# Kernel tuning notes

Measured on AMD Instinct MI355X. Metric: run time of the kernel, lower is better.

The kernel has to match this reference:

```python
import jax, jax.numpy as jnp
import numpy as np

T_EPS = 1e-07
NUM_CAPSULE = 10
DIM_CAPSULE = 64
ROUTINGS = 5


def squash(x, axis=-1):
    # NOTE: this repo's 'squash' is just norm-division (no s/(1+s) factor)
    s = jnp.sum(x * x, axis=axis, keepdims=True)
    return x / jnp.sqrt(s + T_EPS)


def setup_inputs() -> dict:
    key = jax.random.key(0)
    k1, k2 = jax.random.split(key)
    B, N, D = 128, 512, 300
    M = NUM_CAPSULE * DIM_CAPSULE  # 640
    x = jax.random.normal(k1, (B, N, D), dtype=jnp.float32)
    # xavier_normal for shape (1, D, M): std = sqrt(2/(fan_in+fan_out))
    std = float(np.sqrt(2.0 / (D + M)))
    W = jax.random.normal(k2, (1, D, M), dtype=jnp.float32) * std
    return {"x": x, "W": W}


def reference(x, W):
    B, N, D = x.shape
    # u_hat_vecs: [B, num_capsule(i), input_num_capsule(j), dim_capsule(k)]
    u = jnp.einsum('bnd,dm->bnm', x, W[0])
    u = u.reshape(B, N, NUM_CAPSULE, DIM_CAPSULE).transpose(0, 2, 1, 3)
    b = jnp.zeros((B, NUM_CAPSULE, N), dtype=x.dtype)
    outputs = None
    for i in range(ROUTINGS):
        # softmax over the num_capsule axis (axis=1 of b), matching the
        # permute(0,2,1) -> softmax(dim=2) -> permute back in torch
        c = jax.nn.softmax(b, axis=1)
        outputs = squash(jnp.einsum('bij,bijk->bik', c, u))  # [B, num, dim]
        if i < ROUTINGS - 1:
            b = jnp.einsum('bik,bijk->bij', outputs, u)
    return outputs
```

## Files before the change

### kernel.cpp

```cpp
#include <hip/hip_runtime.h>
#include <hip/hip_bf16.h>
#include <stdint.h>

#define BQ 128
#define NJ 512
#define DD 300
#define NC 10
#define DC 64
#define MM 640
#define KP 320
#define RT 5

typedef __attribute__((ext_vector_type(8))) short short8;
typedef __attribute__((ext_vector_type(4))) float f32x4;


__global__ void k_cast_x(const float* __restrict__ x, __hip_bfloat16* __restrict__ xb) {
    int g = blockIdx.x * 256 + threadIdx.x;
    int row = g / 40, cg2 = g - row * 40;
    const float* src = x + (size_t)row * DD + cg2 * 8;
    float4 a = make_float4(0.f, 0.f, 0.f, 0.f), b4 = a;
    if (cg2 < 37) { a = *(const float4*)src; b4 = *(const float4*)(src + 4); }
    else if (cg2 == 37) { a = *(const float4*)src; }
    union { ushort u[8]; uint4 v; } o;
    float f[8] = {a.x, a.y, a.z, a.w, b4.x, b4.y, b4.z, b4.w};
#pragma unroll
    for (int e = 0; e < 8; ++e) {
        __hip_bfloat16 hh = __float2bfloat16(f[e]);
        o.u[e] = *(ushort*)&hh;
    }
    *(uint4*)(xb + (size_t)row * KP + cg2 * 8) = o.v;
}

__global__ void k_cast_w(const float* __restrict__ w, __hip_bfloat16* __restrict__ wt) {
    int idx = blockIdx.x * 256 + threadIdx.x;
    int m = idx / KP, k = idx - m * KP;
    float v = (k < DD) ? w[(size_t)k * MM + m] : 0.f;
    wt[idx] = __float2bfloat16(v);
}

__global__ void k_zero(float4* __restrict__ p) {
    p[blockIdx.x * 256 + threadIdx.x] = make_float4(0.f, 0.f, 0.f, 0.f);
}


__global__ __launch_bounds__(256)
void k_gemm(const __hip_bfloat16* __restrict__ A,
            const __hip_bfloat16* __restrict__ Bt,
            __hip_bfloat16* __restrict__ C,
            float* __restrict__ su) {
    __shared__ __align__(16) __hip_bfloat16 As[128 * 64];
    __shared__ __align__(16) __hip_bfloat16 Bs[128 * 64];

    const int L  = blockIdx.x;
    const int n0 = ((L >> 3) % 5) * 128;
    const int m0 = ((L / 40) * 8 + (L & 7)) * 128;
    const int t  = threadIdx.x;
    const int w  = t >> 6, lane = t & 63;
    const int wrow = (w >> 1) * 64, wcol = (w & 1) * 64;
    const int quad = lane >> 4, r = lane & 15;

    f32x4 acc[4][4] = {};

    const int srow = t >> 3;
    const int sl   = (t & 7) ^ (srow & 7);
    const __hip_bfloat16* ag = A  + (size_t)(m0 + srow) * KP + sl * 8;
    const __hip_bfloat16* bg = Bt + (size_t)(n0 + srow) * KP + sl * 8;

    for (int kt = 0; kt < KP / 64; ++kt) {
        __syncthreads();
#pragma unroll
        for (int s = 0; s < 4; ++s) {
            __builtin_amdgcn_global_load_lds(
                (const __attribute__((address_space(1))) void*)(ag + (size_t)s * 32 * KP + kt * 64),
                (__attribute__((address_space(3))) void*)(&As[s * 2048 + t * 8]), 16, 0, 0);
            __builtin_amdgcn_global_load_lds(
                (const __attribute__((address_space(1))) void*)(bg + (size_t)s * 32 * KP + kt * 64),
                (__attribute__((address_space(3))) void*)(&Bs[s * 2048 + t * 8]), 16, 0, 0);
        }
        __syncthreads();

#pragma unroll
        for (int hh = 0; hh < 2; ++hh) {
            short8 af[4], bf[4];
#pragma unroll
            for (int mi = 0; mi < 4; ++mi) {
                int rho = wrow + mi * 16 + r;
                int p = (hh * 4 + quad) ^ (rho & 7);
                af[mi] = *(const short8*)&As[rho * 64 + p * 8];
            }
#pragma unroll
            for (int ni = 0; ni < 4; ++ni) {
                int rho = wcol + ni * 16 + r;
                int p = (hh * 4 + quad) ^ (rho & 7);
                bf[ni] = *(const short8*)&Bs[rho * 64 + p * 8];
            }
#pragma unroll
            for (int mi = 0; mi < 4; ++mi)
#pragma unroll
                for (int ni = 0; ni < 4; ++ni)
                    acc[mi][ni] = __builtin_amdgcn_mfma_f32_16x16x32_bf16(
                        af[mi], bf[ni], acc[mi][ni], 0, 0, 0);
        }
    }

#pragma unroll
    for (int mi = 0; mi < 4; ++mi)
#pragma unroll
        for (int ni = 0; ni < 4; ++ni) {
            int col = n0 + wcol + ni * 16 + r;
#pragma unroll
            for (int p = 0; p < 4; ++p) {
                int row = m0 + wrow + mi * 16 + quad * 4 + p;
                C[(size_t)row * MM + col] = __float2bfloat16(acc[mi][ni][p]);
            }
        }

    float cs[4];
#pragma unroll
    for (int ni = 0; ni < 4; ++ni) {
        float s = 0.f;
#pragma unroll
        for (int mi = 0; mi < 4; ++mi)
#pragma unroll
            for (int p = 0; p < 4; ++p) s += acc[mi][ni][p];
        s += __shfl_xor(s, 16, 64);
        s += __shfl_xor(s, 32, 64);
        cs[ni] = s;
    }
    if (quad == 0) {
        int bb = m0 >> 9;
#pragma unroll
        for (int ni = 0; ni < 4; ++ni)
            atomicAdd(&su[(size_t)bb * MM + n0 + wcol + ni * 16 + r], cs[ni]);
    }
}


__global__ __launch_bounds__(512)
void k_pass(const __hip_bfloat16* __restrict__ u, const float* __restrict__ pprev,
            float* __restrict__ pnext, int first) {
    __shared__ __align__(16) float outl[MM];
    __shared__ __align__(16) float pored[8 * 32 * 20];

    const int t   = threadIdx.x;
    const int blk = blockIdx.x;
    const int b   = blk >> 2, q = blk & 3;
    const int w   = t >> 6, lane = t & 63;
    const int jd  = t >> 5, kg = t & 31;

    const ushort* ubase = (const ushort*)u
        + (size_t)(b * NJ + q * 128 + jd) * MM + kg * 2;

    uint uv[10];
#pragma unroll
    for (int i = 0; i < 10; ++i) uv[i] = *(const uint*)(ubase + i * 64);

    if (w < 5) {
        float s0, s1;
        if (first) {
            s0 = 0.1f * pprev[(size_t)b * MM + w * 64 + lane];
            s1 = 0.1f * pprev[(size_t)b * MM + 320 + w * 64 + lane];
        } else {
            const float* pp = pprev + (size_t)b * 4 * MM;
            s0 = 0.f; s1 = 0.f;
#pragma unroll
            for (int qq = 0; qq < 4; ++qq) {
                s0 += pp[qq * MM + w * 64 + lane];
                s1 += pp[qq * MM + 320 + w * 64 + lane];
            }
        }
        float q0 = s0 * s0, q1 = s1 * s1;
#pragma unroll
        for (int m = 32; m >= 1; m >>= 1) {
            q0 += __shfl_xor(q0, m, 64);
            q1 += __shfl_xor(q1, m, 64);
        }
        outl[w * 64 + lane]       = s0 * rsqrtf(q0 + 1e-7f);
        outl[320 + w * 64 + lane] = s1 * rsqrtf(q1 + 1e-7f);
    }
    __syncthreads();

    float2 oo[10];
#pragma unroll
    for (int i = 0; i < 10; ++i) oo[i] = *(const float2*)(&outl[i * 64 + kg * 2]);

    float po[20];
#pragma unroll
    for (int e = 0; e < 20; ++e) po[e] = 0.f;

    for (int tt = 0; tt < 8; ++tt) {
        uint nv[10];
        if (tt < 7) {
            const ushort* nrow = ubase + (size_t)(tt + 1) * 16 * MM;
#pragma unroll
            for (int i = 0; i < 10; ++i) nv[i] = *(const uint*)(nrow + i * 64);
        }

        float bl[10];
#pragma unroll
        for (int i = 0; i < 10; ++i) {
            float u0 = __uint_as_float(uv[i] << 16);
            float u1 = __uint_as_float(uv[i] & 0xffff0000u);
            bl[i] = u0 * oo[i].x + u1 * oo[i].y;
        }
#pragma unroll
        for (int m = 1; m <= 16; m <<= 1)
#pragma unroll
            for (int i = 0; i < 10; ++i) bl[i] += __shfl_xor(bl[i], m, 64);

        float mx = -1e30f;
#pragma unroll
        for (int i = 0; i < 10; ++i) mx = fmaxf(mx, bl[i]);
        float ssum = 0.f;
#pragma unroll
        for (int i = 0; i < 10; ++i) { bl[i] = __expf(bl[i] - mx); ssum += bl[i]; }
        float inv = 1.f / ssum;

#pragma unroll
        for (int i = 0; i < 10; ++i) {
            float cc = bl[i] * inv;
            float u0 = __uint_as_float(uv[i] << 16);
            float u1 = __uint_as_float(uv[i] & 0xffff0000u);
            po[i * 2 + 0] += cc * u0;
            po[i * 2 + 1] += cc * u1;
        }

        if (tt < 7) {
#pragma unroll
            for (int i = 0; i < 10; ++i) uv[i] = nv[i];
        }
    }

#pragma unroll
    for (int e = 0; e < 20; ++e) po[e] += __shfl_xor(po[e], 32, 64);
    if (lane < 32) {
#pragma unroll
        for (int e = 0; e < 20; ++e) pored[(w * 32 + kg) * 20 + e] = po[e];
    }
    __syncthreads();
    for (int m = t; m < MM; m += 512) {
        int i = m >> 6, k = m & 63, kg2 = k >> 1, kd = k & 1;
        float s = 0.f;
#pragma unroll
        for (int ww = 0; ww < 8; ++ww) s += pored[(ww * 32 + kg2) * 20 + i * 2 + kd];
        pnext[(size_t)blk * MM + m] = s;
    }
}

__global__ __launch_bounds__(640)
void k_squash(const float* __restrict__ pbuf, float* __restrict__ dst) {
    int b = blockIdx.x, t = threadIdx.x;
    float s = 0.f;
#pragma unroll
    for (int qq = 0; qq < 4; ++qq) s += pbuf[(size_t)(b * 4 + qq) * MM + t];
    float sq = s * s;
#pragma unroll
    for (int m = 32; m >= 1; m >>= 1) sq += __shfl_xor(sq, m, 64);
    dst[(size_t)b * MM + t] = s * rsqrtf(sq + 1e-7f);
}


extern "C" void kernel_launch(void* const* d_in, const int* in_sizes, int n_in,
                              void* d_out, int out_size, void* d_ws, size_t ws_size,
                              hipStream_t stream) {
    const float* x = (const float*)d_in[0];
    const float* W = (const float*)d_in[1];
    float* out = (float*)d_out;

    char* ws = (char*)d_ws;
    size_t o = 0;
    __hip_bfloat16* xb = (__hip_bfloat16*)(ws + o); o += (size_t)BQ * NJ * KP * 2;
    __hip_bfloat16* wt = (__hip_bfloat16*)(ws + o); o += (size_t)MM * KP * 2;
    __hip_bfloat16* u  = (__hip_bfloat16*)(ws + o); o += (size_t)BQ * NJ * MM * 2;
    float* pb0 = (float*)(ws + o); o += (size_t)512 * MM * 4;
    float* pb1 = (float*)(ws + o); o += (size_t)512 * MM * 4;
    float* su  = (float*)(ws + o); o += (size_t)BQ * MM * 4;

    k_cast_x<<<(BQ * NJ * 40) / 256, 256, 0, stream>>>(x, xb);
    k_cast_w<<<(MM * KP) / 256, 256, 0, stream>>>(W, wt);
    k_zero<<<(BQ * MM) / (4 * 256), 256, 0, stream>>>((float4*)su);
    k_gemm<<<2560, 256, 0, stream>>>(xb, wt, u, su);

    k_pass<<<512, 512, 0, stream>>>(u, su,  pb0, 1);
    k_pass<<<512, 512, 0, stream>>>(u, pb0, pb1, 0);
    k_pass<<<512, 512, 0, stream>>>(u, pb1, pb0, 0);
    k_pass<<<512, 512, 0, stream>>>(u, pb0, pb1, 0);
    k_squash<<<BQ, 640, 0, stream>>>(pb1, out);
}
```

Baseline: 255.1 us.

## Split routing passes into finer blocks with separate combine/squash kernels

Each routing pass now runs as 2048 blocks of 256 threads, each covering 32 input capsules, instead of 512 blocks of 512 threads covering 128. The partial-sum combine and squash move out of the pass kernel into a small standalone kernel that runs between passes. The goal is more blocks for better occupancy and latency hiding on the memory-bound u streaming. In exchange there are four extra kernel launches, more partial sums to reduce, and more scattered traffic on the partial buffer.

```diff
diff --git a/kernel.cpp b/kernel.cpp
--- a/kernel.cpp
+++ b/kernel.cpp
@@ -137,62 +137,50 @@
 }
 
 
-__global__ __launch_bounds__(512)
-void k_pass(const __hip_bfloat16* __restrict__ u, const float* __restrict__ pprev,
-            float* __restrict__ pnext, int first) {
-    __shared__ __align__(16) float outl[MM];
-    __shared__ __align__(16) float pored[8 * 32 * 20];
+__global__ __launch_bounds__(640)
+void k_comb(const float* __restrict__ src, float* __restrict__ dst,
+            int nsrc, float scale) {
+    int b = blockIdx.x, t = threadIdx.x;
+    float s = 0.f;
+    for (int q = 0; q < nsrc; ++q) s += src[(size_t)(b * nsrc + q) * MM + t];
+    s *= scale;
+    float sq = s * s;
+#pragma unroll
+    for (int m = 32; m >= 1; m >>= 1) sq += __shfl_xor(sq, m, 64);
+    dst[(size_t)b * MM + t] = s * rsqrtf(sq + 1e-7f);
+}
+
+
+__global__ __launch_bounds__(256, 5)
+void k_pass(const __hip_bfloat16* __restrict__ u, const float* __restrict__ out,
+            float* __restrict__ pnext) {
+    __shared__ __align__(16) float pored[4 * 32 * 20];
 
     const int t   = threadIdx.x;
     const int blk = blockIdx.x;
-    const int b   = blk >> 2, q = blk & 3;
-    const int w   = t >> 6, lane = t & 63;
+    const int b   = blk >> 4, six = blk & 15;
+    const int w   = t >> 6;
     const int jd  = t >> 5, kg = t & 31;
 
     const ushort* ubase = (const ushort*)u
-        + (size_t)(b * NJ + q * 128 + jd) * MM + kg * 2;
+        + (size_t)(b * NJ + six * 32 + jd) * MM + kg * 2;
 
     uint uv[10];
 #pragma unroll
     for (int i = 0; i < 10; ++i) uv[i] = *(const uint*)(ubase + i * 64);
 
-    if (w < 5) {
-        float s0, s1;
-        if (first) {
-            s0 = 0.1f * pprev[(size_t)b * MM + w * 64 + lane];
-            s1 = 0.1f * pprev[(size_t)b * MM + 320 + w * 64 + lane];
-        } else {
-            const float* pp = pprev + (size_t)b * 4 * MM;
-            s0 = 0.f; s1 = 0.f;
-#pragma unroll
-            for (int qq = 0; qq < 4; ++qq) {
-                s0 += pp[qq * MM + w * 64 + lane];
-                s1 += pp[qq * MM + 320 + w * 64 + lane];
-            }
-        }
-        float q0 = s0 * s0, q1 = s1 * s1;
-#pragma unroll
-        for (int m = 32; m >= 1; m >>= 1) {
-            q0 += __shfl_xor(q0, m, 64);
-            q1 += __shfl_xor(q1, m, 64);
-        }
-        outl[w * 64 + lane]       = s0 * rsqrtf(q0 + 1e-7f);
-        outl[320 + w * 64 + lane] = s1 * rsqrtf(q1 + 1e-7f);
-    }
-    __syncthreads();
-
     float2 oo[10];
 #pragma unroll
-    for (int i = 0; i < 10; ++i) oo[i] = *(const float2*)(&outl[i * 64 + kg * 2]);
+    for (int i = 0; i < 10; ++i) oo[i] = *(const float2*)(out + (size_t)b * MM + i * 64 + kg * 2);
 
     float po[20];
 #pragma unroll
     for (int e = 0; e < 20; ++e) po[e] = 0.f;
 
-    for (int tt = 0; tt < 8; ++tt) {
+    for (int tt = 0; tt < 4; ++tt) {
         uint nv[10];
-        if (tt < 7) {
-            const ushort* nrow = ubase + (size_t)(tt + 1) * 16 * MM;
+        if (tt < 3) {
+            const ushort* nrow = ubase + (size_t)(tt + 1) * 8 * MM;
 #pragma unroll
             for (int i = 0; i < 10; ++i) nv[i] = *(const uint*)(nrow + i * 64);
         }
@@ -226,7 +214,7 @@
             po[i * 2 + 1] += cc * u1;
         }
 
-        if (tt < 7) {
+        if (tt < 3) {
 #pragma unroll
             for (int i = 0; i < 10; ++i) uv[i] = nv[i];
         }
@@ -234,30 +222,18 @@
 
 #pragma unroll
     for (int e = 0; e < 20; ++e) po[e] += __shfl_xor(po[e], 32, 64);
-    if (lane < 32) {
+    if ((t & 63) < 32) {
 #pragma unroll
         for (int e = 0; e < 20; ++e) pored[(w * 32 + kg) * 20 + e] = po[e];
     }
     __syncthreads();
-    for (int m = t; m < MM; m += 512) {
+    for (int m = t; m < MM; m += 256) {
         int i = m >> 6, k = m & 63, kg2 = k >> 1, kd = k & 1;
         float s = 0.f;
 #pragma unroll
-        for (int ww = 0; ww < 8; ++ww) s += pored[(ww * 32 + kg2) * 20 + i * 2 + kd];
+        for (int ww = 0; ww < 4; ++ww) s += pored[(ww * 32 + kg2) * 20 + i * 2 + kd];
         pnext[(size_t)blk * MM + m] = s;
     }
-}
-
-__global__ __launch_bounds__(640)
-void k_squash(const float* __restrict__ pbuf, float* __restrict__ dst) {
-    int b = blockIdx.x, t = threadIdx.x;
-    float s = 0.f;
-#pragma unroll
-    for (int qq = 0; qq < 4; ++qq) s += pbuf[(size_t)(b * 4 + qq) * MM + t];
-    float sq = s * s;
-#pragma unroll
-    for (int m = 32; m >= 1; m >>= 1) sq += __shfl_xor(sq, m, 64);
-    dst[(size_t)b * MM + t] = s * rsqrtf(sq + 1e-7f);
 }
 
 
@@ -273,8 +249,8 @@
     __hip_bfloat16* xb = (__hip_bfloat16*)(ws + o); o += (size_t)BQ * NJ * KP * 2;
     __hip_bfloat16* wt = (__hip_bfloat16*)(ws + o); o += (size_t)MM * KP * 2;
     __hip_bfloat16* u  = (__hip_bfloat16*)(ws + o); o += (size_t)BQ * NJ * MM * 2;
-    float* pb0 = (float*)(ws + o); o += (size_t)512 * MM * 4;
-    float* pb1 = (float*)(ws + o); o += (size_t)512 * MM * 4;
+    float* pb  = (float*)(ws + o); o += (size_t)2048 * MM * 4;
+    float* ob  = (float*)(ws + o); o += (size_t)BQ * MM * 4;
     float* su  = (float*)(ws + o); o += (size_t)BQ * MM * 4;
 
     k_cast_x<<<(BQ * NJ * 40) / 256, 256, 0, stream>>>(x, xb);
@@ -282,9 +258,13 @@
     k_zero<<<(BQ * MM) / (4 * 256), 256, 0, stream>>>((float4*)su);
     k_gemm<<<2560, 256, 0, stream>>>(xb, wt, u, su);
 
-    k_pass<<<512, 512, 0, stream>>>(u, su,  pb0, 1);
-    k_pass<<<512, 512, 0, stream>>>(u, pb0, pb1, 0);
-    k_pass<<<512, 512, 0, stream>>>(u, pb1, pb0, 0);
-    k_pass<<<512, 512, 0, stream>>>(u, pb0, pb1, 0);
-    k_squash<<<BQ, 640, 0, stream>>>(pb1, out);
-}
+    k_comb<<<BQ, 640, 0, stream>>>(su, ob, 1, 0.1f);
+    k_pass<<<2048, 256, 0, stream>>>(u, ob, pb);
+    k_comb<<<BQ, 640, 0, stream>>>(pb, ob, 16, 1.f);
+    k_pass<<<2048, 256, 0, stream>>>(u, ob, pb);
+    k_comb<<<BQ, 640, 0, stream>>>(pb, ob, 16, 1.f);
+    k_pass<<<2048, 256, 0, stream>>>(u, ob, pb);
+    k_comb<<<BQ, 640, 0, stream>>>(pb, ob, 16, 1.f);
+    k_pass<<<2048, 256, 0, stream>>>(u, ob, pb);
+    k_comb<<<BQ, 640, 0, stream>>>(pb, out, 16, 1.f);
+}
```

New measurement: 280.4 us. +9.9%, slower.
